# Optimization experiments

Hardware: AMD Instinct MI355X
Metric: run time of the kernel (lower is better)

The kernel has to match this reference:

```python
import jax, jax.numpy as jnp
import numpy as np

B, L, D = 2, 2048, 1024
H, HD = 16, 64   # num_heads, head_dim
LD = 256         # mla latent dim


def setup_inputs() -> dict:
    key = jax.random.key(0)
    ks = jax.random.split(key, 6)
    s = lambda fan_in: 1.0 / np.sqrt(fan_in)
    x_bld = jax.random.normal(ks[0], (B, L, D), dtype=jnp.float32)
    Wq = jax.random.normal(ks[1], (D, H, HD), dtype=jnp.float32) * s(D)
    Wkv_down = jax.random.normal(ks[2], (D, LD), dtype=jnp.float32) * s(D)
    Wk_up = jax.random.normal(ks[3], (LD, H, HD), dtype=jnp.float32) * s(LD)
    Wv_up = jax.random.normal(ks[4], (LD, H, HD), dtype=jnp.float32) * s(LD)
    Wout = jax.random.normal(ks[5], (H, HD, D), dtype=jnp.float32) * s(H * HD)
    return {"x_bld": x_bld, "Wq": Wq, "Wkv_down": Wkv_down,
            "Wk_up": Wk_up, "Wv_up": Wv_up, "Wout": Wout}


def reference(x_bld, Wq, Wkv_down, Wk_up, Wv_up, Wout):
    # projections
    q_blhd = jnp.einsum('bld,dhk->blhk', x_bld, Wq)
    latent_bll = jnp.einsum('bld,dc->blc', x_bld, Wkv_down)   # [B,L,LD]
    k_blhd = jnp.einsum('blc,chk->blhk', latent_bll, Wk_up)
    v_blhd = jnp.einsum('blc,chk->blhk', latent_bll, Wv_up)
    # attention scores [B,H,L,L]
    attn = jnp.einsum('bqhd,bkhd->bhqk', q_blhd, k_blhd) / jnp.sqrt(
        jnp.asarray(HD, dtype=x_bld.dtype))
    # causal mask (no window)
    l = x_bld.shape[1]
    mask = (jnp.arange(l)[None, :] <= jnp.arange(l)[:, None])[None, None]
    neg_inf = jnp.finfo(attn.dtype).min
    attn = jax.nn.softmax(jnp.where(mask, attn, neg_inf), axis=-1)
    y_blhd = jnp.einsum('bhqk,bkhd->bqhd', attn, v_blhd)
    return jnp.einsum('bqhd,hdo->bqo', y_blhd, Wout)
```

## Files before the change

### kernel.cpp

```cpp
#include <hip/hip_runtime.h>
#include <hip/hip_bf16.h>

#define BB   2
#define LL   2048
#define DD   1024
#define HH   16
#define HDD  64
#define LDIM 256
#define MTOT (BB * LL)

using short8  = __attribute__((ext_vector_type(8))) short;
using floatx4 = __attribute__((ext_vector_type(4))) float;

static __device__ __forceinline__ unsigned short f2bf(float x) {
  __hip_bfloat16 h = __float2bfloat16(x);
  return *reinterpret_cast<unsigned short*>(&h);
}
static __device__ __forceinline__ unsigned int pk_bf16(float a, float b) {
  return (unsigned int)f2bf(a) | ((unsigned int)f2bf(b) << 16);
}
static __device__ __forceinline__ void load_lds16(const unsigned short* g,
                                                  unsigned short* l) {
  __builtin_amdgcn_global_load_lds(
      (const __attribute__((address_space(1))) unsigned int*)g,
      (__attribute__((address_space(3))) unsigned int*)l, 16, 0, 0);
}
template <int N>
static __device__ __forceinline__ void waitcnt_vm() {
  if constexpr (N == 0) asm volatile("s_waitcnt vmcnt(0)" ::: "memory");
  else if constexpr (N == 4) asm volatile("s_waitcnt vmcnt(4)" ::: "memory");
  else if constexpr (N == 6) asm volatile("s_waitcnt vmcnt(6)" ::: "memory");
  else if constexpr (N == 8) asm volatile("s_waitcnt vmcnt(8)" ::: "memory");
}
static __device__ __forceinline__ void lds_drain_barrier() {
  asm volatile("s_waitcnt lgkmcnt(0)\n\ts_barrier" ::: "memory");
}

__global__ __launch_bounds__(256) void cast_bf16(const float* __restrict__ in,
                                                 unsigned short* __restrict__ out,
                                                 int n4) {
  const int i = (blockIdx.x * 256 + threadIdx.x);
  if (i < n4) {
    float4 v = ((const float4*)in)[i];
    ushort4 o;
    o.x = f2bf(v.x); o.y = f2bf(v.y); o.z = f2bf(v.z); o.w = f2bf(v.w);
    ((ushort4*)out)[i] = o;
  }
}

__global__ __launch_bounds__(256) void transpose_cast5(
    const float* __restrict__ Wq, const float* __restrict__ Wkv,
    const float* __restrict__ Wku, const float* __restrict__ Wvu,
    const float* __restrict__ Wo,
    unsigned short* __restrict__ WqT, unsigned short* __restrict__ WkvT,
    unsigned short* __restrict__ WkuT, unsigned short* __restrict__ WvuT,
    unsigned short* __restrict__ WoT) {
  const float* src; unsigned short* dst; int R, C;
  switch (blockIdx.z) {
    case 0:  src = Wq;  dst = WqT;  R = 1024; C = 1024; break;
    case 1:  src = Wkv; dst = WkvT; R = 1024; C = 256;  break;
    case 2:  src = Wku; dst = WkuT; R = 256;  C = 1024; break;
    case 3:  src = Wvu; dst = WvuT; R = 256;  C = 1024; break;
    default: src = Wo;  dst = WoT;  R = 1024; C = 1024; break;
  }
  if ((int)blockIdx.x * 32 >= C || (int)blockIdx.y * 32 >= R) return;

  __shared__ float tile[32][33];
  const int tx = threadIdx.x, ty = threadIdx.y;
#pragma unroll
  for (int i = 0; i < 4; ++i) {
    const int r = blockIdx.y * 32 + ty + i * 8;
    tile[ty + i * 8][tx] = src[(size_t)r * C + blockIdx.x * 32 + tx];
  }
  __syncthreads();
#pragma unroll
  for (int i = 0; i < 4; ++i) {
    const int c = blockIdx.x * 32 + ty + i * 8;
    dst[(size_t)c * R + blockIdx.y * 32 + tx] = f2bf(tile[tx][ty + i * 8]);
  }
}

template <int KIND, int BMT, int BNT, int BKT>
__global__ __launch_bounds__(256) void gemm2(const unsigned short* __restrict__ A,
                                             const unsigned short* __restrict__ Bt0,
                                             const unsigned short* __restrict__ Bt1,
                                             void* __restrict__ C0,
                                             void* __restrict__ C1,
                                             int M, int N, int K, int nsplit) {
  constexpr int IM = BMT / 32, JN = BNT / 32;
  constexpr int TA = BMT * BKT, TB = BNT * BKT;
  constexpr int NIA = TA / 2048, NIB = TB / 2048;
  constexpr int NLD = NIA + NIB;
  constexpr int RPI = 2048 / BKT;
  __shared__ __align__(16) unsigned short As[2 * TA];
  __shared__ __align__(16) unsigned short Bs[2 * TB];

  const int tid  = threadIdx.x;
  const int w    = tid >> 6;
  const int lane = tid & 63;
  const int lo   = lane & 15;
  const int g    = lane >> 4;
  const int wr   = w >> 1, wc = w & 1;
  const int row0  = blockIdx.x * BMT;
  const int col0g = blockIdx.y * BNT;
  const bool second = (col0g >= nsplit);
  const unsigned short* Btp = second ? Bt1 : Bt0;
  const int col0 = second ? col0g - nsplit : col0g;

  floatx4 acc[IM][JN];
#pragma unroll
  for (int i = 0; i < IM; ++i)
#pragma unroll
    for (int j = 0; j < JN; ++j) acc[i][j] = (floatx4){0.f, 0.f, 0.f, 0.f};

  const int sr = (BKT == 32) ? (tid >> 2) : (tid >> 3);
  const int sc = (BKT == 32) ? (tid & 3) : (tid & 7);

  auto swz = [](int chunk, int row) {
    if constexpr (BKT == 32) return chunk ^ ((row >> 1) & 3);
    else                     return chunk ^ (row & 7);
  };

  auto stage = [&](int buf, int k0) {
#pragma unroll
    for (int inst = 0; inst < NIA; ++inst) {
      const int r  = inst * RPI + sr;
      const int cs = swz(sc, r);
      load_lds16(A + (size_t)(row0 + r) * K + k0 + cs * 8,
                 As + buf * TA + inst * 2048 + w * 512);
    }
#pragma unroll
    for (int inst = 0; inst < NIB; ++inst) {
      const int r  = inst * RPI + sr;
      const int cs = swz(sc, r);
      load_lds16(Btp + (size_t)(col0 + r) * K + k0 + cs * 8,
                 Bs + buf * TB + inst * 2048 + w * 512);
    }
  };

  const int nk = K / BKT;
  stage(0, 0);
  for (int it = 0; it < nk; ++it) {
    const int cur = it & 1;
    if (it + 1 < nk) {
      stage(cur ^ 1, (it + 1) * BKT);
      waitcnt_vm<NLD>();
    } else {
      waitcnt_vm<0>();
    }
    asm volatile("s_barrier" ::: "memory");

    const unsigned short* Ac = As + cur * TA;
    const unsigned short* Bc = Bs + cur * TB;
#pragma unroll
    for (int kk = 0; kk < BKT / 32; ++kk) {
      short8 af[IM], bf[JN];
#pragma unroll
      for (int i = 0; i < IM; ++i) {
        const int rm = (BMT / 2) * wr + 16 * i + lo;
        af[i] = *(const short8*)(Ac + (size_t)rm * BKT + swz(kk * 4 + g, rm) * 8);
      }
#pragma unroll
      for (int j = 0; j < JN; ++j) {
        const int rn = (BNT / 2) * wc + 16 * j + lo;
        bf[j] = *(const short8*)(Bc + (size_t)rn * BKT + swz(kk * 4 + g, rn) * 8);
      }
#pragma unroll
      for (int i = 0; i < IM; ++i)
#pragma unroll
        for (int j = 0; j < JN; ++j)
          acc[i][j] = __builtin_amdgcn_mfma_f32_16x16x32_bf16(af[i], bf[j], acc[i][j], 0, 0, 0);
    }

    lds_drain_barrier();
  }

#pragma unroll
  for (int i = 0; i < IM; ++i) {
    const int mbase = row0 + (BMT / 2) * wr + 16 * i + g * 4;
#pragma unroll
    for (int j = 0; j < JN; ++j) {
      const int nl = col0 + (BNT / 2) * wc + 16 * j + lo;
      const int bq = mbase >> 11, hh = nl >> 6, d = nl & 63;
      if (KIND == 2 && second) {
        const int l = mbase & 2047;
        uint2 o;
        o.x = pk_bf16(acc[i][j][0], acc[i][j][1]);
        o.y = pk_bf16(acc[i][j][2], acc[i][j][3]);
        *(uint2*)(&((unsigned short*)C1)[((size_t)(bq * HH + hh) * HDD + d) * LL + l]) = o;
      } else {
#pragma unroll
        for (int r = 0; r < 4; ++r) {
          const float v = acc[i][j][r];
          const int mm = mbase + r;
          const int l = mm & 2047;
          if (KIND == 0) {
            ((float*)C0)[(size_t)mm * N + nl] = v;
          } else if (KIND == 1) {
            if (!second)
              ((unsigned short*)C0)[((size_t)(bq * HH + hh) * LL + l) * HDD + d] = f2bf(v);
            else
              ((unsigned short*)C1)[(size_t)mm * LDIM + nl] = f2bf(v);
          } else {
            ((unsigned short*)C0)[((size_t)(bq * HH + hh) * LL + l) * HDD + d] = f2bf(v);
          }
        }
      }
    }
  }
}

#define SC2 0.18033688011112042f

__global__ __launch_bounds__(256) void flash_mfma9(const unsigned short* __restrict__ Qh,
                                                   const unsigned short* __restrict__ Kh,
                                                   const unsigned short* __restrict__ Vt,
                                                   unsigned short* __restrict__ y) {
  const int w    = threadIdx.x >> 6;
  const int lane = threadIdx.x & 63;
  const int lo   = lane & 15;
  const int g    = lane >> 4;
  const int h    = blockIdx.x;
  const int b    = blockIdx.y;
  const int pair = blockIdx.z;
  const int qtH  = 31 - pair;
  const int qtL  = pair;

  __shared__ __align__(16) unsigned short Ks[3 * 64 * 64];
  __shared__ __align__(16) unsigned short Vs[3 * 64 * 64];
  __shared__ __align__(16) unsigned short Pq[4][2][16 * 64];

  const size_t bh = (size_t)(b * HH + h);
  const unsigned short* Qp = Qh + bh * LL * HDD;
  const unsigned short* Kp = Kh + bh * LL * HDD;
  const unsigned short* Vp = Vt + bh * (size_t)HDD * LL;
  unsigned short* PwH = Pq[w][0];
  unsigned short* PwL = Pq[w][1];

  const int qHw = qtH * 64 + w * 16;
  const int qLw = qtL * 64 + w * 16;

  short8 qfH0 = *(const short8*)(Qp + (size_t)(qHw + lo) * HDD + g * 8);
  short8 qfH1 = *(const short8*)(Qp + (size_t)(qHw + lo) * HDD + 32 + g * 8);
  short8 qfL0 = *(const short8*)(Qp + (size_t)(qLw + lo) * HDD + g * 8);
  short8 qfL1 = *(const short8*)(Qp + (size_t)(qLw + lo) * HDD + 32 + g * 8);

  floatx4 otH[4], otL[4];
#pragma unroll
  for (int ds = 0; ds < 4; ++ds) {
    otH[ds] = (floatx4){0.f, 0.f, 0.f, 0.f};
    otL[ds] = (floatx4){0.f, 0.f, 0.f, 0.f};
  }
  float lsumH = 0.f, lsumL = 0.f;

  const int srow = lane >> 3;
  const int sch  = lane & 7;

  auto stage = [&](int buf, int k0) {
#pragma unroll
    for (int t = 0; t < 2; ++t) {
      const int rbase = w * 16 + t * 8;
      const int row   = rbase + srow;
      const int cs    = sch ^ (row & 7);
      load_lds16(Kp + (size_t)(k0 + row) * HDD + cs * 8, Ks + buf * 4096 + rbase * 64);
      load_lds16(Vp + (size_t)row * LL + k0 + cs * 8,    Vs + buf * 4096 + rbase * 64);
    }
  };

  auto qk = [&](const unsigned short* Kc, short8 q0f, short8 q1f, floatx4* st) {
#pragma unroll
    for (int ks = 0; ks < 4; ++ks) {
      const int rm = ks * 16 + lo;
      short8 a0 = *(const short8*)(Kc + rm * 64 + ((g ^ (rm & 7)) * 8));
      short8 a1 = *(const short8*)(Kc + rm * 64 + (((4 + g) ^ (rm & 7)) * 8));
      floatx4 s = (floatx4){0.f, 0.f, 0.f, 0.f};
      s = __builtin_amdgcn_mfma_f32_16x16x32_bf16(a0, q0f, s, 0, 0, 0);
      s = __builtin_amdgcn_mfma_f32_16x16x32_bf16(a1, q1f, s, 0, 0, 0);
      st[ks] = s;
    }
  };
  auto sm = [&](floatx4* st, unsigned short* P, float& lsum, int qw, int k0,
                bool masked) {
    if (!masked) {
#pragma unroll
      for (int ks = 0; ks < 4; ++ks) {
        float p[4];
#pragma unroll
        for (int r = 0; r < 4; ++r) {
          p[r] = __builtin_amdgcn_exp2f(st[ks][r] * SC2);
          lsum += p[r];
        }
        uint2 w2;
        w2.x = pk_bf16(p[0], p[1]);
        w2.y = pk_bf16(p[2], p[3]);
        *(uint2*)(P + lo * 64 + (((ks * 2 + (g >> 1)) ^ (lo & 7)) * 8) + (g & 1) * 4) = w2;
      }
    } else {
      const int qq = qw + lo;
#pragma unroll
      for (int ks = 0; ks < 4; ++ks) {
        float p[4];
#pragma unroll
        for (int r = 0; r < 4; ++r) {
          const int kk = k0 + ks * 16 + g * 4 + r;
          const float e = __builtin_amdgcn_exp2f(st[ks][r] * SC2);
          p[r] = (kk <= qq) ? e : 0.f;
          lsum += p[r];
        }
        uint2 w2;
        w2.x = pk_bf16(p[0], p[1]);
        w2.y = pk_bf16(p[2], p[3]);
        *(uint2*)(P + lo * 64 + (((ks * 2 + (g >> 1)) ^ (lo & 7)) * 8) + (g & 1) * 4) = w2;
      }
    }
  };
  auto pv = [&](const unsigned short* Vc, const unsigned short* P, floatx4* ot) {
    short8 pf0 = *(const short8*)(P + lo * 64 + ((g ^ (lo & 7)) * 8));
    short8 pf1 = *(const short8*)(P + lo * 64 + (((4 + g) ^ (lo & 7)) * 8));
#pragma unroll
    for (int ds = 0; ds < 4; ++ds) {
      const int rm = ds * 16 + lo;
      short8 v0 = *(const short8*)(Vc + rm * 64 + ((g ^ (rm & 7)) * 8));
      short8 v1 = *(const short8*)(Vc + rm * 64 + (((4 + g) ^ (rm & 7)) * 8));
      ot[ds] = __builtin_amdgcn_mfma_f32_16x16x32_bf16(v0, pf0, ot[ds], 0, 0, 0);
      ot[ds] = __builtin_amdgcn_mfma_f32_16x16x32_bf16(v1, pf1, ot[ds], 0, 0, 0);
    }
  };

  const int ntiles = qtH + 1;
  stage(0, 0);
  stage(1, 64);
  for (int it = 0; it < ntiles; ++it) {
    const int cur = it % 3;
    const int k0  = it * 64;
    if (it + 2 < ntiles) {
      stage((it + 2) % 3, k0 + 128);
      waitcnt_vm<8>();
    } else if (it + 1 < ntiles) {
      waitcnt_vm<4>();
    } else {
      waitcnt_vm<0>();
    }
    asm volatile("s_barrier" ::: "memory");

    const unsigned short* Kc = Ks + cur * 4096;
    const unsigned short* Vc = Vs + cur * 4096;
    const bool doL = (it <= qtL);

    floatx4 stH[4], stL[4];
    qk(Kc, qfH0, qfH1, stH);
    if (doL) qk(Kc, qfL0, qfL1, stL);
    sm(stH, PwH, lsumH, qHw, k0, it == qtH);
    if (doL) sm(stL, PwL, lsumL, qLw, k0, it == qtL);
    pv(Vc, PwH, otH);
    if (doL) pv(Vc, PwL, otL);

    lds_drain_barrier();
  }

  auto finish = [&](floatx4* ot, float lsum, int qw) {
    float s = lsum;
    s += __shfl_xor(s, 16);
    s += __shfl_xor(s, 32);
    const float inv = 1.0f / s;
#pragma unroll
    for (int ds = 0; ds < 4; ++ds) {
      uint2 o;
      o.x = pk_bf16(ot[ds][0] * inv, ot[ds][1] * inv);
      o.y = pk_bf16(ot[ds][2] * inv, ot[ds][3] * inv);
      *(uint2*)(y + (size_t)(b * LL + qw + lo) * (HH * HDD) + h * HDD + ds * 16 + g * 4) = o;
    }
  };
  finish(otH, lsumH, qHw);
  finish(otL, lsumL, qLw);
}

extern "C" void kernel_launch(void* const* d_in, const int* in_sizes, int n_in,
                              void* d_out, int out_size, void* d_ws, size_t ws_size,
                              hipStream_t stream) {
  const float* x   = (const float*)d_in[0];
  const float* Wq  = (const float*)d_in[1];
  const float* Wkv = (const float*)d_in[2];
  const float* Wku = (const float*)d_in[3];
  const float* Wvu = (const float*)d_in[4];
  const float* Wo  = (const float*)d_in[5];
  float* out = (float*)d_out;

  unsigned short* xb     = (unsigned short*)d_ws;
  unsigned short* WqT    = xb + (size_t)MTOT * DD;
  unsigned short* WkvT   = WqT + 1024 * 1024;
  unsigned short* WkuT   = WkvT + 256 * 1024;
  unsigned short* WvuT   = WkuT + 1024 * 256;
  unsigned short* WoT    = WvuT + 1024 * 256;
  unsigned short* latent = WoT + 1024 * 1024;
  unsigned short* Qh     = latent + (size_t)MTOT * LDIM;
  unsigned short* Kh     = Qh + (size_t)MTOT * DD;
  unsigned short* Vt     = Kh + (size_t)MTOT * DD;
  unsigned short* y      = Vt + (size_t)MTOT * DD;

  cast_bf16<<<dim3(MTOT * DD / 1024), dim3(256), 0, stream>>>(x, xb, MTOT * DD / 4);
  transpose_cast5<<<dim3(32, 32, 5), dim3(32, 8), 0, stream>>>(
      Wq, Wkv, Wku, Wvu, Wo, WqT, WkvT, WkuT, WvuT, WoT);

  gemm2<1, 128, 64, 64><<<dim3(MTOT / 128, 1280 / 64), dim3(256), 0, stream>>>(
      xb, WqT, WkvT, Qh, latent, MTOT, 1280, DD, 1024);
  gemm2<2, 128, 128, 32><<<dim3(MTOT / 128, 2048 / 128), dim3(256), 0, stream>>>(
      latent, WkuT, WvuT, Kh, Vt, MTOT, 2048, LDIM, 1024);

  flash_mfma9<<<dim3(HH, BB, 16), dim3(256), 0, stream>>>(Qh, Kh, Vt, y);

  gemm2<0, 128, 64, 64><<<dim3(MTOT / 128, DD / 64), dim3(256), 0, stream>>>(
      y, WoT, nullptr, out, nullptr, MTOT, DD, DD, DD);
}
```

Measured before the change: 169.1 us.

## Split flash attention key tiles across two wave groups per block

The flash kernel now runs 512 threads per block. Two groups of four waves each take one half of every 64-key tile, so each wave does half the QK, softmax and PV work per tile. Partial outputs and row sums are combined through shared memory at the end. This is meant to raise wave-level parallelism and hide latency, since the grid is only 512 blocks. The cost is an extra reduction step and a synchronisation barrier, plus more waves competing for the same LDS.

```diff
diff --git a/kernel.cpp b/kernel.cpp
--- a/kernel.cpp
+++ b/kernel.cpp
@@ -28,6 +28,7 @@
 template <int N>
 static __device__ __forceinline__ void waitcnt_vm() {
   if constexpr (N == 0) asm volatile("s_waitcnt vmcnt(0)" ::: "memory");
+  else if constexpr (N == 2) asm volatile("s_waitcnt vmcnt(2)" ::: "memory");
   else if constexpr (N == 4) asm volatile("s_waitcnt vmcnt(4)" ::: "memory");
   else if constexpr (N == 6) asm volatile("s_waitcnt vmcnt(6)" ::: "memory");
   else if constexpr (N == 8) asm volatile("s_waitcnt vmcnt(8)" ::: "memory");
@@ -212,14 +213,16 @@
 
 #define SC2 0.18033688011112042f
 
-__global__ __launch_bounds__(256) void flash_mfma9(const unsigned short* __restrict__ Qh,
-                                                   const unsigned short* __restrict__ Kh,
-                                                   const unsigned short* __restrict__ Vt,
-                                                   unsigned short* __restrict__ y) {
+__global__ __launch_bounds__(512, 4) void flash_mfma10(const unsigned short* __restrict__ Qh,
+                                                       const unsigned short* __restrict__ Kh,
+                                                       const unsigned short* __restrict__ Vt,
+                                                       unsigned short* __restrict__ y) {
   const int w    = threadIdx.x >> 6;
   const int lane = threadIdx.x & 63;
   const int lo   = lane & 15;
   const int g    = lane >> 4;
+  const int kw   = w >> 2;
+  const int wq   = w & 3;
   const int h    = blockIdx.x;
   const int b    = blockIdx.y;
   const int pair = blockIdx.z;
@@ -228,7 +231,7 @@
 
   __shared__ __align__(16) unsigned short Ks[3 * 64 * 64];
   __shared__ __align__(16) unsigned short Vs[3 * 64 * 64];
-  __shared__ __align__(16) unsigned short Pq[4][2][16 * 64];
+  __shared__ __align__(16) unsigned short Pq[8][2][16 * 32];
 
   const size_t bh = (size_t)(b * HH + h);
   const unsigned short* Qp = Qh + bh * LL * HDD;
@@ -237,8 +240,8 @@
   unsigned short* PwH = Pq[w][0];
   unsigned short* PwL = Pq[w][1];
 
-  const int qHw = qtH * 64 + w * 16;
-  const int qLw = qtL * 64 + w * 16;
+  const int qHw = qtH * 64 + wq * 16;
+  const int qLw = qtL * 64 + wq * 16;
 
   short8 qfH0 = *(const short8*)(Qp + (size_t)(qHw + lo) * HDD + g * 8);
   short8 qfH1 = *(const short8*)(Qp + (size_t)(qHw + lo) * HDD + 32 + g * 8);
@@ -257,20 +260,16 @@
   const int sch  = lane & 7;
 
   auto stage = [&](int buf, int k0) {
-#pragma unroll
-    for (int t = 0; t < 2; ++t) {
-      const int rbase = w * 16 + t * 8;
-      const int row   = rbase + srow;
-      const int cs    = sch ^ (row & 7);
-      load_lds16(Kp + (size_t)(k0 + row) * HDD + cs * 8, Ks + buf * 4096 + rbase * 64);
-      load_lds16(Vp + (size_t)row * LL + k0 + cs * 8,    Vs + buf * 4096 + rbase * 64);
-    }
+    const int row = w * 8 + srow;
+    const int cs  = sch ^ (row & 7);
+    load_lds16(Kp + (size_t)(k0 + row) * HDD + cs * 8, Ks + buf * 4096 + w * 512);
+    load_lds16(Vp + (size_t)row * LL + k0 + cs * 8,    Vs + buf * 4096 + w * 512);
   };
 
   auto qk = [&](const unsigned short* Kc, short8 q0f, short8 q1f, floatx4* st) {
 #pragma unroll
-    for (int ks = 0; ks < 4; ++ks) {
-      const int rm = ks * 16 + lo;
+    for (int ks = 0; ks < 2; ++ks) {
+      const int rm = kw * 32 + ks * 16 + lo;
       short8 a0 = *(const short8*)(Kc + rm * 64 + ((g ^ (rm & 7)) * 8));
       short8 a1 = *(const short8*)(Kc + rm * 64 + (((4 + g) ^ (rm & 7)) * 8));
       floatx4 s = (floatx4){0.f, 0.f, 0.f, 0.f};
@@ -283,7 +282,7 @@
                 bool masked) {
     if (!masked) {
 #pragma unroll
-      for (int ks = 0; ks < 4; ++ks) {
+      for (int ks = 0; ks < 2; ++ks) {
         float p[4];
 #pragma unroll
         for (int r = 0; r < 4; ++r) {
@@ -293,16 +292,16 @@
         uint2 w2;
         w2.x = pk_bf16(p[0], p[1]);
         w2.y = pk_bf16(p[2], p[3]);
-        *(uint2*)(P + lo * 64 + (((ks * 2 + (g >> 1)) ^ (lo & 7)) * 8) + (g & 1) * 4) = w2;
+        *(uint2*)(P + lo * 32 + (((ks * 2 + (g >> 1)) ^ (lo & 3)) * 8) + (g & 1) * 4) = w2;
       }
     } else {
       const int qq = qw + lo;
 #pragma unroll
-      for (int ks = 0; ks < 4; ++ks) {
+      for (int ks = 0; ks < 2; ++ks) {
         float p[4];
 #pragma unroll
         for (int r = 0; r < 4; ++r) {
-          const int kk = k0 + ks * 16 + g * 4 + r;
+          const int kk = k0 + kw * 32 + ks * 16 + g * 4 + r;
           const float e = __builtin_amdgcn_exp2f(st[ks][r] * SC2);
           p[r] = (kk <= qq) ? e : 0.f;
           lsum += p[r];
@@ -310,20 +309,17 @@
         uint2 w2;
         w2.x = pk_bf16(p[0], p[1]);
         w2.y = pk_bf16(p[2], p[3]);
-        *(uint2*)(P + lo * 64 + (((ks * 2 + (g >> 1)) ^ (lo & 7)) * 8) + (g & 1) * 4) = w2;
+        *(uint2*)(P + lo * 32 + (((ks * 2 + (g >> 1)) ^ (lo & 3)) * 8) + (g & 1) * 4) = w2;
       }
     }
   };
   auto pv = [&](const unsigned short* Vc, const unsigned short* P, floatx4* ot) {
-    short8 pf0 = *(const short8*)(P + lo * 64 + ((g ^ (lo & 7)) * 8));
-    short8 pf1 = *(const short8*)(P + lo * 64 + (((4 + g) ^ (lo & 7)) * 8));
+    short8 pf = *(const short8*)(P + lo * 32 + ((g ^ (lo & 3)) * 8));
 #pragma unroll
     for (int ds = 0; ds < 4; ++ds) {
       const int rm = ds * 16 + lo;
-      short8 v0 = *(const short8*)(Vc + rm * 64 + ((g ^ (rm & 7)) * 8));
-      short8 v1 = *(const short8*)(Vc + rm * 64 + (((4 + g) ^ (rm & 7)) * 8));
-      ot[ds] = __builtin_amdgcn_mfma_f32_16x16x32_bf16(v0, pf0, ot[ds], 0, 0, 0);
-      ot[ds] = __builtin_amdgcn_mfma_f32_16x16x32_bf16(v1, pf1, ot[ds], 0, 0, 0);
+      short8 v = *(const short8*)(Vc + rm * 64 + (((kw * 4 + g) ^ (rm & 7)) * 8));
+      ot[ds] = __builtin_amdgcn_mfma_f32_16x16x32_bf16(v, pf, ot[ds], 0, 0, 0);
     }
   };
 
@@ -335,9 +331,9 @@
     const int k0  = it * 64;
     if (it + 2 < ntiles) {
       stage((it + 2) % 3, k0 + 128);
-      waitcnt_vm<8>();
+      waitcnt_vm<4>();
     } else if (it + 1 < ntiles) {
-      waitcnt_vm<4>();
+      waitcnt_vm<2>();
     } else {
       waitcnt_vm<0>();
     }
@@ -347,7 +343,7 @@
     const unsigned short* Vc = Vs + cur * 4096;
     const bool doL = (it <= qtL);
 
-    floatx4 stH[4], stL[4];
+    floatx4 stH[2], stL[2];
     qk(Kc, qfH0, qfH1, stH);
     if (doL) qk(Kc, qfL0, qfL1, stL);
     sm(stH, PwH, lsumH, qHw, k0, it == qtH);
@@ -358,21 +354,48 @@
     lds_drain_barrier();
   }
 
-  auto finish = [&](floatx4* ot, float lsum, int qw) {
-    float s = lsum;
-    s += __shfl_xor(s, 16);
-    s += __shfl_xor(s, 32);
-    const float inv = 1.0f / s;
+  float sH = lsumH; sH += __shfl_xor(sH, 16); sH += __shfl_xor(sH, 32);
+  float sL = lsumL; sL += __shfl_xor(sL, 16); sL += __shfl_xor(sL, 32);
+  float* oshH = (float*)Ks;
+  float* oshL = (float*)Vs;
+  float* lsh  = (float*)&Pq[0][0][0];
+
+  if (kw == 1) {
+    const int base = (wq * 64 + lane) * 16;
 #pragma unroll
     for (int ds = 0; ds < 4; ++ds) {
-      uint2 o;
-      o.x = pk_bf16(ot[ds][0] * inv, ot[ds][1] * inv);
-      o.y = pk_bf16(ot[ds][2] * inv, ot[ds][3] * inv);
-      *(uint2*)(y + (size_t)(b * LL + qw + lo) * (HH * HDD) + h * HDD + ds * 16 + g * 4) = o;
-    }
-  };
-  finish(otH, lsumH, qHw);
-  finish(otL, lsumL, qLw);
+      *(floatx4*)(oshH + base + ds * 4) = otH[ds];
+      *(floatx4*)(oshL + base + ds * 4) = otL[ds];
+    }
+    if (lane < 16) {
+      lsh[wq * 16 + lane]      = sH;
+      lsh[64 + wq * 16 + lane] = sL;
+    }
+  }
+  __syncthreads();
+  if (kw == 0) {
+    const int base = (wq * 64 + lane) * 16;
+#pragma unroll
+    for (int ds = 0; ds < 4; ++ds) {
+      otH[ds] += *(const floatx4*)(oshH + base + ds * 4);
+      otL[ds] += *(const floatx4*)(oshL + base + ds * 4);
+    }
+    sH += lsh[wq * 16 + lo];
+    sL += lsh[64 + wq * 16 + lo];
+
+    auto finish = [&](floatx4* ot, float stot, int qw) {
+      const float inv = 1.0f / stot;
+#pragma unroll
+      for (int ds = 0; ds < 4; ++ds) {
+        uint2 o;
+        o.x = pk_bf16(ot[ds][0] * inv, ot[ds][1] * inv);
+        o.y = pk_bf16(ot[ds][2] * inv, ot[ds][3] * inv);
+        *(uint2*)(y + (size_t)(b * LL + qw + lo) * (HH * HDD) + h * HDD + ds * 16 + g * 4) = o;
+      }
+    };
+    finish(otH, sH, qHw);
+    finish(otL, sL, qLw);
+  }
 }
 
 extern "C" void kernel_launch(void* const* d_in, const int* in_sizes, int n_in,
@@ -407,7 +430,7 @@
   gemm2<2, 128, 128, 32><<<dim3(MTOT / 128, 2048 / 128), dim3(256), 0, stream>>>(
       latent, WkuT, WvuT, Kh, Vt, MTOT, 2048, LDIM, 1024);
 
-  flash_mfma9<<<dim3(HH, BB, 16), dim3(256), 0, stream>>>(Qh, Kh, Vt, y);
+  flash_mfma10<<<dim3(HH, BB, 16), dim3(512), 0, stream>>>(Qh, Kh, Vt, y);
 
   gemm2<0, 128, 64, 64><<<dim3(MTOT / 128, DD / 64), dim3(256), 0, stream>>>(
       y, WoT, nullptr, out, nullptr, MTOT, DD, DD, DD);
```

After: 164.3 us. -2.8%, faster.
